# Kernel optimization log

Measured on AMD Instinct MI355X. Metric: run time of the kernel, lower is better.

Reference implementation:

```python
import jax, jax.numpy as jnp
import numpy as np

N_ATOMS = 1_000_000
DESC_DIM = 128
HIDDEN = 128
N_ELEM = 4  # element ids 0..3


def setup_inputs() -> dict:
    key = jax.random.key(0)
    ks = jax.random.split(key, 6)
    element = jax.random.randint(ks[0], (N_ATOMS,), 0, N_ELEM, dtype=jnp.int32)
    desc = jax.random.normal(ks[1], (N_ATOMS, DESC_DIM), dtype=jnp.float32)
    # Per-element MLP experts: desc_dim -> hidden -> 1
    W1 = jax.random.normal(ks[2], (N_ELEM, DESC_DIM, HIDDEN), dtype=jnp.float32) / np.sqrt(DESC_DIM)
    b1 = jnp.zeros((N_ELEM, HIDDEN), dtype=jnp.float32)
    W2 = jax.random.normal(ks[3], (N_ELEM, HIDDEN), dtype=jnp.float32) / np.sqrt(HIDDEN)
    b2 = jnp.zeros((N_ELEM,), dtype=jnp.float32)
    return {"element": element, "desc": desc, "W1": W1, "b1": b1, "W2": W2, "b2": b2}


def reference(element, desc, W1, b1, W2, b2):
    """Per-element dispatch: each atom's descriptor goes through the MLP for
    its atomic number. JAX jit needs static shapes, so we compute each
    expert densely and select with where (loop over small fixed expert set)."""
    out = jnp.zeros(desc.shape[0], dtype=desc.dtype)
    for e in range(W1.shape[0]):
        h = jax.nn.relu(desc @ W1[e] + b1[e])      # [N, HIDDEN]
        y = h @ W2[e] + b2[e]                       # [N]
        out = jnp.where(element == e, y, out)
    return out
```

## Files before the change

kernel.cpp:

```cpp
#include <hip/hip_runtime.h>
#include <hip/hip_bf16.h>

typedef __attribute__((ext_vector_type(8))) short short8;
typedef __attribute__((ext_vector_type(4))) float float4v;

__device__ __forceinline__ unsigned short f2bf(float f) {
    unsigned int u = __float_as_uint(f);
    u += 0x7fffu + ((u >> 16) & 1u);
    return (unsigned short)(u >> 16);
}

__global__ void count_kernel(const int* __restrict__ elem, int n, int* __restrict__ bc) {
    const int t = threadIdx.x, b = blockIdx.x;
    const int base = b * 1024;
    int c[4] = {0, 0, 0, 0};
    #pragma unroll
    for (int i = 0; i < 4; ++i) {
        const int a = base + i * 256 + t;
        if (a < n) c[elem[a]]++;
    }
    int p0 = c[0] | (c[1] << 16);
    int p1 = c[2] | (c[3] << 16);
    #pragma unroll
    for (int off = 1; off < 64; off <<= 1) { p0 += __shfl_xor(p0, off); p1 += __shfl_xor(p1, off); }
    __shared__ int wsum[4][4];
    const int w = t >> 6, lane = t & 63;
    if (lane == 0) {
        wsum[w][0] = p0 & 0xffff; wsum[w][1] = p0 >> 16;
        wsum[w][2] = p1 & 0xffff; wsum[w][3] = p1 >> 16;
    }
    __syncthreads();
    if (t < 4) {
        int s = 0;
        #pragma unroll
        for (int ww = 0; ww < 4; ++ww) s += wsum[ww][t];
        bc[b * 4 + t] = s;
    }
}

__global__ void scan_kernel(int* __restrict__ bc, int* __restrict__ offs, int nb) {
    const int t = threadIdx.x, w = t >> 6, lane = t & 63;
    int vals[16];
    int s = 0;
    #pragma unroll
    for (int j = 0; j < 16; ++j) {
        const int i = lane * 16 + j;
        const int v = (i < nb) ? bc[i * 4 + w] : 0;
        vals[j] = s; s += v;
    }
    int incl = s;
    #pragma unroll
    for (int off = 1; off < 64; off <<= 1) {
        const int v = __shfl_up(incl, off);
        if (lane >= off) incl += v;
    }
    const int excl = incl - s;
    __shared__ int tot[4];
    __shared__ int eoff[4];
    if (lane == 63) tot[w] = incl;
    __syncthreads();
    if (t == 0) {
        int a = 0;
        for (int e = 0; e < 4; ++e) { eoff[e] = a; offs[e] = a; a += tot[e]; }
        offs[4] = a;
    }
    __syncthreads();
    const int myoff = eoff[w] + excl;
    #pragma unroll
    for (int j = 0; j < 16; ++j) {
        const int i = lane * 16 + j;
        if (i < nb) bc[i * 4 + w] = myoff + vals[j];
    }
}

__global__ void scatter_kernel(const int* __restrict__ elem, int n,
                               const int* __restrict__ bc, int* __restrict__ idx_sorted) {
    const int t = threadIdx.x, b = blockIdx.x;
    const int w = t >> 6, lane = t & 63;
    const int base = b * 1024;
    int ev[4];
    #pragma unroll
    for (int i = 0; i < 4; ++i) {
        const int a = base + i * 256 + t;
        ev[i] = (a < n) ? elem[a] : -1;
    }
    __shared__ int tbl[4][4][4];
    __shared__ int sbase[4];
    #pragma unroll
    for (int i = 0; i < 4; ++i) {
        #pragma unroll
        for (int el = 0; el < 4; ++el) {
            const unsigned long long m = __ballot(ev[i] == el);
            if (lane == 0) tbl[i][w][el] = (int)__popcll(m);
        }
    }
    if (t < 4) sbase[t] = bc[b * 4 + t];
    __syncthreads();
    if (t < 4) {
        int s = 0;
        for (int i = 0; i < 4; ++i)
            for (int w2 = 0; w2 < 4; ++w2) { const int v = tbl[i][w2][t]; tbl[i][w2][t] = s; s += v; }
    }
    __syncthreads();
    #pragma unroll
    for (int i = 0; i < 4; ++i) {
        unsigned long long m[4];
        #pragma unroll
        for (int el = 0; el < 4; ++el) m[el] = __ballot(ev[i] == el);
        const int a = base + i * 256 + t;
        if (a < n) {
            const int el = ev[i];
            const int rank = (int)__popcll(m[el] & ((1ull << lane) - 1ull));
            idx_sorted[sbase[el] + tbl[i][w][el] + rank] = a;
        }
    }
}

__global__ void w1t_kernel(const float* __restrict__ W1, unsigned short* __restrict__ W1T) {
    const int b = blockIdx.x;
    const int e = b >> 7, nn = b & 127;
    const int k = threadIdx.x;
    const float v = W1[((size_t)(e * 128 + k)) * 128 + nn];
    W1T[((size_t)(e * 128 + nn)) * 128 + k] = f2bf(v);
}

__global__ __launch_bounds__(256, 2)
void expert_mlp_kernel(const float* __restrict__ desc,
                       const unsigned short* __restrict__ W1T,
                       const float* __restrict__ b1,
                       const float* __restrict__ W2,
                       const float* __restrict__ b2,
                       const int* __restrict__ idx_sorted,
                       const int* __restrict__ offs,
                       float* __restrict__ out) {
    __shared__ unsigned short As[128 * 128];
    __shared__ unsigned short Bs[128 * 128];

    const int bx = blockIdx.x;
    const int e = bx & 3;
    const int tile = bx >> 2;
    const int base = offs[e];
    const int cnt = offs[e + 1] - base;
    const int m0 = tile * 128;
    if (m0 >= cnt) return;
    const int t = threadIdx.x;

    {
        const uint4* src = (const uint4*)(W1T + (size_t)e * 16384);
        const int c = t & 15, nrow = t >> 4;
        #pragma unroll
        for (int p = 0; p < 8; ++p) {
            const int nn = nrow + p * 16;
            const uint4 v = src[nn * 16 + c];
            const int pc = c ^ (nn & 7);
            *(uint4*)(&Bs[nn * 128 + pc * 8]) = v;
        }
    }
    {
        const int c = t & 31, rr = t >> 5;
        #pragma unroll
        for (int p = 0; p < 16; ++p) {
            const int r = p * 8 + rr;
            const int gm = m0 + r;
            const int gi = idx_sorted[base + ((gm < cnt) ? gm : 0)];
            const float4 v = *(const float4*)(desc + (size_t)gi * 128 + c * 4);
            ushort4 pk;
            pk.x = f2bf(v.x); pk.y = f2bf(v.y); pk.z = f2bf(v.z); pk.w = f2bf(v.w);
            const int pc = (c >> 1) ^ (r & 7);
            *(ushort4*)(&As[r * 128 + pc * 8 + (c & 1) * 4]) = pk;
        }
    }
    __syncthreads();

    const int lane = t & 63;
    const int wv = t >> 6;
    const int quad = lane >> 4;
    const int l16 = lane & 15;
    const int mbase = wv * 32;
    const int r7 = l16 & 7;

    float4v acc[2][8] = {};
    #pragma unroll
    for (int ks = 0; ks < 4; ++ks) {
        const int pco = ((ks * 4 + quad) ^ r7) * 8;
        const short8 a0 = *(const short8*)(&As[(mbase + l16) * 128 + pco]);
        const short8 a1 = *(const short8*)(&As[(mbase + 16 + l16) * 128 + pco]);
        #pragma unroll
        for (int nt = 0; nt < 8; ++nt) {
            const short8 bf = *(const short8*)(&Bs[(nt * 16 + l16) * 128 + pco]);
            acc[0][nt] = __builtin_amdgcn_mfma_f32_16x16x32_bf16(a0, bf, acc[0][nt], 0, 0, 0);
            acc[1][nt] = __builtin_amdgcn_mfma_f32_16x16x32_bf16(a1, bf, acc[1][nt], 0, 0, 0);
        }
    }

    float b1v[8], w2v[8];
    #pragma unroll
    for (int nt = 0; nt < 8; ++nt) {
        b1v[nt] = b1[e * 128 + nt * 16 + l16];
        w2v[nt] = W2[e * 128 + nt * 16 + l16];
    }
    const float b2e = b2[e];
    #pragma unroll
    for (int mt = 0; mt < 2; ++mt) {
        float y[4] = {0.f, 0.f, 0.f, 0.f};
        #pragma unroll
        for (int nt = 0; nt < 8; ++nt) {
            const float4v v = acc[mt][nt];
            #pragma unroll
            for (int r = 0; r < 4; ++r)
                y[r] += fmaxf(v[r] + b1v[nt], 0.f) * w2v[nt];
        }
        #pragma unroll
        for (int off = 1; off < 16; off <<= 1) {
            #pragma unroll
            for (int r = 0; r < 4; ++r) y[r] += __shfl_xor(y[r], off, 16);
        }
        if (l16 == 0) {
            #pragma unroll
            for (int r = 0; r < 4; ++r) {
                const int m = mbase + mt * 16 + quad * 4 + r;
                const int gm = m0 + m;
                if (gm < cnt) out[idx_sorted[base + gm]] = y[r] + b2e;
            }
        }
    }
}

extern "C" void kernel_launch(void* const* d_in, const int* in_sizes, int n_in,
                              void* d_out, int out_size, void* d_ws, size_t ws_size,
                              hipStream_t stream) {
    const int*   elem = (const int*)d_in[0];
    const float* desc = (const float*)d_in[1];
    const float* W1   = (const float*)d_in[2];
    const float* b1   = (const float*)d_in[3];
    const float* W2   = (const float*)d_in[4];
    const float* b2   = (const float*)d_in[5];
    float* out = (float*)d_out;
    const int n = in_sizes[0];

    char* ws = (char*)d_ws;
    int* bc         = (int*)ws;
    int* offs       = (int*)(ws + 16128);
    int* idx_sorted = (int*)(ws + 16384);
    unsigned short* W1T = (unsigned short*)(ws + 16384 + (size_t)n * 4);

    const int nb = (n + 1023) / 1024;
    count_kernel  <<<nb, 256, 0, stream>>>(elem, n, bc);
    scan_kernel   <<<1, 256, 0, stream>>>(bc, offs, nb);
    scatter_kernel<<<nb, 256, 0, stream>>>(elem, n, bc, idx_sorted);
    w1t_kernel    <<<512, 128, 0, stream>>>(W1, W1T);

    const int tiles = (n + 127) / 128;
    expert_mlp_kernel<<<tiles * 4, 256, 0, stream>>>(desc, W1T, b1, W2, b2, idx_sorted, offs, out);
}
```

Baseline: 691.5 us.

## Load MFMA operands directly from global memory, dropping LDS staging

Removes the shared-memory tiles for descriptors and transposed weights. Each lane now gathers its own descriptor rows and W1T fragments straight from global memory into MFMA registers, converting to bf16 on the fly, and the block-wide barrier goes away. Launch bounds are raised to 3 blocks per SM since LDS no longer limits occupancy. The trade-off is that W1T fragments are re-read from global/L2 by every wave with no reuse across waves, and the gather loads land directly on the MFMA critical path with no staging to hide latency.

```diff
diff --git a/kernel.cpp b/kernel.cpp
--- a/kernel.cpp
+++ b/kernel.cpp
@@ -124,7 +124,7 @@
     W1T[((size_t)(e * 128 + nn)) * 128 + k] = f2bf(v);
 }
 
-__global__ __launch_bounds__(256, 2)
+__global__ __launch_bounds__(256, 3)
 void expert_mlp_kernel(const float* __restrict__ desc,
                        const unsigned short* __restrict__ W1T,
                        const float* __restrict__ b1,
@@ -133,9 +133,6 @@
                        const int* __restrict__ idx_sorted,
                        const int* __restrict__ offs,
                        float* __restrict__ out) {
-    __shared__ unsigned short As[128 * 128];
-    __shared__ unsigned short Bs[128 * 128];
-
     const int bx = blockIdx.x;
     const int e = bx & 3;
     const int tile = bx >> 2;
@@ -143,51 +140,43 @@
     const int cnt = offs[e + 1] - base;
     const int m0 = tile * 128;
     if (m0 >= cnt) return;
+
     const int t = threadIdx.x;
-
-    {
-        const uint4* src = (const uint4*)(W1T + (size_t)e * 16384);
-        const int c = t & 15, nrow = t >> 4;
-        #pragma unroll
-        for (int p = 0; p < 8; ++p) {
-            const int nn = nrow + p * 16;
-            const uint4 v = src[nn * 16 + c];
-            const int pc = c ^ (nn & 7);
-            *(uint4*)(&Bs[nn * 128 + pc * 8]) = v;
-        }
-    }
-    {
-        const int c = t & 31, rr = t >> 5;
-        #pragma unroll
-        for (int p = 0; p < 16; ++p) {
-            const int r = p * 8 + rr;
-            const int gm = m0 + r;
-            const int gi = idx_sorted[base + ((gm < cnt) ? gm : 0)];
-            const float4 v = *(const float4*)(desc + (size_t)gi * 128 + c * 4);
-            ushort4 pk;
-            pk.x = f2bf(v.x); pk.y = f2bf(v.y); pk.z = f2bf(v.z); pk.w = f2bf(v.w);
-            const int pc = (c >> 1) ^ (r & 7);
-            *(ushort4*)(&As[r * 128 + pc * 8 + (c & 1) * 4]) = pk;
-        }
-    }
-    __syncthreads();
-
     const int lane = t & 63;
     const int wv = t >> 6;
     const int quad = lane >> 4;
     const int l16 = lane & 15;
     const int mbase = wv * 32;
-    const int r7 = l16 & 7;
+
+    const int gm0 = m0 + mbase + l16;
+    const int gm1 = gm0 + 16;
+    const int cl = cnt - 1;
+    const int gi0 = idx_sorted[base + (gm0 < cl ? gm0 : cl)];
+    const int gi1 = idx_sorted[base + (gm1 < cl ? gm1 : cl)];
+
+    const float* arow0 = desc + (size_t)gi0 * 128 + quad * 8;
+    const float* arow1 = desc + (size_t)gi1 * 128 + quad * 8;
+    const unsigned short* brow = W1T + (size_t)e * 16384 + l16 * 128 + quad * 8;
 
     float4v acc[2][8] = {};
     #pragma unroll
     for (int ks = 0; ks < 4; ++ks) {
-        const int pco = ((ks * 4 + quad) ^ r7) * 8;
-        const short8 a0 = *(const short8*)(&As[(mbase + l16) * 128 + pco]);
-        const short8 a1 = *(const short8*)(&As[(mbase + 16 + l16) * 128 + pco]);
+        const float4 fa0 = *(const float4*)(arow0 + ks * 32);
+        const float4 fb0 = *(const float4*)(arow0 + ks * 32 + 4);
+        const float4 fa1 = *(const float4*)(arow1 + ks * 32);
+        const float4 fb1 = *(const float4*)(arow1 + ks * 32 + 4);
+        short8 a0, a1;
+        a0[0] = (short)f2bf(fa0.x); a0[1] = (short)f2bf(fa0.y);
+        a0[2] = (short)f2bf(fa0.z); a0[3] = (short)f2bf(fa0.w);
+        a0[4] = (short)f2bf(fb0.x); a0[5] = (short)f2bf(fb0.y);
+        a0[6] = (short)f2bf(fb0.z); a0[7] = (short)f2bf(fb0.w);
+        a1[0] = (short)f2bf(fa1.x); a1[1] = (short)f2bf(fa1.y);
+        a1[2] = (short)f2bf(fa1.z); a1[3] = (short)f2bf(fa1.w);
+        a1[4] = (short)f2bf(fb1.x); a1[5] = (short)f2bf(fb1.y);
+        a1[6] = (short)f2bf(fb1.z); a1[7] = (short)f2bf(fb1.w);
         #pragma unroll
         for (int nt = 0; nt < 8; ++nt) {
-            const short8 bf = *(const short8*)(&Bs[(nt * 16 + l16) * 128 + pco]);
+            const short8 bf = *(const short8*)(brow + nt * 2048 + ks * 32);
             acc[0][nt] = __builtin_amdgcn_mfma_f32_16x16x32_bf16(a0, bf, acc[0][nt], 0, 0, 0);
             acc[1][nt] = __builtin_amdgcn_mfma_f32_16x16x32_bf16(a1, bf, acc[1][nt], 0, 0, 0);
         }
```

Result: slower. 779.7 us (+12.8%).
